# Kernel tuning notes

Hardware: AMD Instinct MI355X
Metric: run time of the kernel (lower is better)

## Reference

```python
import jax, jax.numpy as jnp
import numpy as np
from jax import lax

EPS = 1e-07
B, H, W = 32, 120, 120
N_PRIM, PRIM_DIM = 16, 8          # 16 capsule types, 8-d pose
N_SEC, SEC_DIM = 10, 16           # 10 secondary capsules, 16-d
FLAT = 9216                       # 16 * 24 * 24
R_ITERS = 3
REC_DIM = H * W * 3               # 43200


def _conv(x, w, b, stride):
    # NHWC input, HWIO kernel, VALID padding
    y = lax.conv_general_dilated(x, w, (stride, stride), 'VALID',
                                 dimension_numbers=('NHWC', 'HWIO', 'NHWC'))
    return y + b


def _squash(s):
    s_norm = jnp.linalg.norm(s, axis=-1, keepdims=True)
    sq = jnp.square(s_norm)
    return sq / (1.0 + sq) * s / (s_norm + EPS)


def setup_inputs() -> dict:
    key = jax.random.key(0)
    ks = jax.random.split(key, 13)
    p = lambda k, shp, s=0.05: (jax.random.normal(k, shp, dtype=jnp.float32) * s)
    inp = {
        'input_x': jax.random.normal(ks[0], (B, H, W, 3), dtype=jnp.float32),
        'y':       jax.random.uniform(ks[1], (B, N_SEC), dtype=jnp.float32),
        'conv1_w': p(ks[2], (9, 9, 3, 256)),
        'conv1_b': jnp.zeros((256,), jnp.float32),
        'conv2_w': p(ks[3], (9, 9, 256, N_PRIM * PRIM_DIM)),
        'conv2_b': jnp.zeros((N_PRIM * PRIM_DIM,), jnp.float32),
        'w_pose':  p(ks[4], (1, FLAT, N_SEC, SEC_DIM, PRIM_DIM)),
        'w1': p(ks[5], (N_SEC * SEC_DIM, 512)), 'b1': jnp.zeros((512,), jnp.float32),
        'w2': p(ks[6], (512, 1024)),            'b2': jnp.zeros((1024,), jnp.float32),
        'w3': p(ks[7], (1024, REC_DIM)),        'b3': jnp.zeros((REC_DIM,), jnp.float32),
    }
    return inp


def reference(input_x, y, conv1_w, conv1_b, conv2_w, conv2_b, w_pose,
              w1, b1, w2, b2, w3, b3):
    b = input_x.shape[0]
    # feature extraction
    x = jax.nn.relu(_conv(input_x, conv1_w, conv1_b, 2))   # [B,56,56,256]
    x = _conv(x, conv2_w, conv2_b, 2)                      # [B,24,24,128]
    u = x.reshape(b, FLAT, PRIM_DIM)                       # [B,9216,8]
    # u_hat[b,n,c,d] = sum_p w_pose[0,n,c,d,p] * u[b,n,p]
    u_hat = jnp.einsum('ncdp,bnp->bncd', w_pose[0], u)     # [B,9216,10,16]
    # dynamic routing
    logits = jnp.zeros((b, FLAT, N_SEC, 1), jnp.float32)
    v = None
    for _ in range(R_ITERS):
        c = jax.nn.softmax(logits, axis=-2)                # over secondary caps
        s = jnp.sum(c * u_hat, axis=1, keepdims=True)      # [B,1,10,16]
        v = _squash(s)
        agreement = jnp.sum(u_hat * v, axis=-1, keepdims=True)  # [B,9216,10,1]
        logits = logits + agreement
    # masking + reconstruction
    mask = y[:, None, :, None]                             # [B,1,10,1]
    v_flat = (mask * v).reshape(b, -1)                     # [B,160]
    h = jax.nn.relu(v_flat @ w1 + b1)
    h = jax.nn.relu(h @ w2 + b2)
    rec = jax.nn.sigmoid(h @ w3 + b3)                      # [B,43200]
    return v, rec
```

## Files before the change

### kernel.cpp

```cpp
#include <hip/hip_runtime.h>
#include <hip/hip_bf16.h>

typedef unsigned short u16;
typedef unsigned int   u32;
typedef __attribute__((ext_vector_type(8))) __bf16 bf16x8;
typedef __attribute__((ext_vector_type(4))) float  f32x4;

#define EPSQ 1e-7f
#define KSPLIT 9
#define KPB 2304
#define KSTEPS 72
#define FC3SPL 8

#define GLDS16(gp, lp) __builtin_amdgcn_global_load_lds( \
    (const __attribute__((address_space(1))) void*)(gp), \
    (__attribute__((address_space(3))) void*)(lp), 16, 0, 0)
#define WAITV4() asm volatile("s_waitcnt vmcnt(4)" ::: "memory")
#define WAITV0() asm volatile("s_waitcnt vmcnt(0)" ::: "memory")

__device__ __forceinline__ u16 f2bf(float f){
  u32 u = __float_as_uint(f);
  u32 r = (u + 0x7fffu + ((u >> 16) & 1u)) >> 16;
  return (u16)r;
}
__device__ __forceinline__ float bf2f(u16 h){ return __uint_as_float(((u32)h) << 16); }
__device__ __forceinline__ float blo(u32 w){ return __uint_as_float(w << 16); }
__device__ __forceinline__ float bhi(u32 w){ return __uint_as_float(w & 0xffff0000u); }

__global__ __launch_bounds__(256) void k_im2col(const float* __restrict__ x, u16* __restrict__ A1){
  const int id = blockIdx.x*256 + threadIdx.x;
  const int m  = id >> 5;
  const int s  = id & 31;
  const int b  = m / 3136;
  const int r  = m - b*3136;
  const int oy = r / 56;
  const int ox = r - oy*56;
  const float* xb = x + ((size_t)b*120 + 2*oy)*120*3 + 2*ox*3;
  u16 vals[8];
  #pragma unroll
  for (int j=0;j<8;++j){
    int k = s*8 + j;
    if (k < 243){
      int ky = k / 27;
      int rem = k - ky*27;
      vals[j] = f2bf(xb[(size_t)ky*360 + rem]);
    } else vals[j] = 0;
  }
  *reinterpret_cast<uint4*>(A1 + (size_t)m*256 + s*8) = *reinterpret_cast<uint4*>(vals);
}

__global__ __launch_bounds__(256) void k_wt1(const float* __restrict__ w, u16* __restrict__ wt){
  __shared__ float tile[32][33];
  const int k0 = blockIdx.x*32;
  const int c0 = blockIdx.y*32;
  const int c  = threadIdx.x & 31;
  const int r8 = threadIdx.x >> 5;
  #pragma unroll
  for (int rr=0; rr<4; ++rr){
    int r = r8*4+rr;
    tile[r][c] = (k0+r < 243) ? w[(size_t)(k0+r)*256 + c0 + c] : 0.f;
  }
  __syncthreads();
  #pragma unroll
  for (int rr=0; rr<4; ++rr){
    int r = r8*4+rr;
    wt[(size_t)(c0+r)*256 + k0 + c] = f2bf(tile[c][r]);
  }
}

__global__ __launch_bounds__(256) void k_gemm1(const u16* __restrict__ A1,
    const u16* __restrict__ w1t, const float* __restrict__ bias, u16* __restrict__ a1b){
  __shared__ __align__(16) u16 As[2][4096];
  __shared__ __align__(16) u16 Bs[2][4096];
  const int t  = threadIdx.x;
  const int bx = blockIdx.x;
  const int by = blockIdx.y;
  const int row0  = t>>2;
  const int sslot = (t&3) ^ ((t>>3)&3);
  const int wid = t>>6, lane = t&63;
  const int wr = wid>>1, wc = wid&1, lr = lane&15, lq = lane>>4;
  const int sl = lq ^ ((lr>>1)&3);
  const size_t srcA0 = (size_t)(bx*128 + row0)*256 + sslot*8;
  const size_t srcA1 = srcA0 + (size_t)64*256;
  const size_t srcB0 = (size_t)(by*128 + row0)*256 + sslot*8;
  const size_t srcB1 = srcB0 + (size_t)64*256;
  f32x4 acc[4][4];
  #pragma unroll
  for (int i=0;i<4;++i)
    #pragma unroll
    for (int j=0;j<4;++j) acc[i][j] = (f32x4){0.f,0.f,0.f,0.f};
  int aoff[4], boff[4];
  #pragma unroll
  for (int i=0;i<4;++i){
    aoff[i] = (wr*64 + i*16 + lr)*32 + sl*8;
    boff[i] = (wc*64 + i*16 + lr)*32 + sl*8;
  }

  auto stage = [&](int step, int buf){
    const int k0 = step*32;
    GLDS16(A1 + srcA0 + k0, &As[buf][wid*512]);
    GLDS16(A1 + srcA1 + k0, &As[buf][wid*512 + 2048]);
    GLDS16(w1t + srcB0 + k0, &Bs[buf][wid*512]);
    GLDS16(w1t + srcB1 + k0, &Bs[buf][wid*512 + 2048]);
  };
  auto compute = [&](int buf){
    bf16x8 af[4], bfv[4];
    #pragma unroll
    for (int mi=0;mi<4;++mi)
      af[mi] = *reinterpret_cast<const bf16x8*>(&As[buf][aoff[mi]]);
    #pragma unroll
    for (int ni=0;ni<4;++ni)
      bfv[ni] = *reinterpret_cast<const bf16x8*>(&Bs[buf][boff[ni]]);
    #pragma unroll
    for (int mi=0;mi<4;++mi)
      #pragma unroll
      for (int ni=0;ni<4;++ni)
        acc[mi][ni] = __builtin_amdgcn_mfma_f32_16x16x32_bf16(af[mi], bfv[ni], acc[mi][ni], 0, 0, 0);
  };

  stage(0, 0);
  int cur = 0;
  for (int step=0; step<8; ++step){
    if (step+1 < 8){
      stage(step+1, cur^1);
      WAITV4();
    } else {
      WAITV0();
    }
    __builtin_amdgcn_s_barrier();
    __builtin_amdgcn_sched_barrier(0);
    compute(cur);
    __builtin_amdgcn_s_barrier();
    __builtin_amdgcn_sched_barrier(0);
    cur ^= 1;
  }

  #pragma unroll
  for (int ni=0;ni<4;++ni){
    int colg = by*128 + wc*64 + ni*16 + lr;
    float bv = bias[colg];
    #pragma unroll
    for (int mi=0;mi<4;++mi){
      #pragma unroll
      for (int r=0;r<4;++r){
        int rowg = bx*128 + wr*64 + mi*16 + lq*4 + r;
        float v = fmaxf(acc[mi][ni][r] + bv, 0.f);
        a1b[(size_t)rowg*256 + colg] = f2bf(v);
      }
    }
  }
}

__global__ __launch_bounds__(256) void k_wt(const float* __restrict__ w, u16* __restrict__ wt){
  __shared__ float tile[32][33];
  const int k0 = blockIdx.x*32;
  const int c0 = blockIdx.y*32;
  const int c  = threadIdx.x & 31;
  const int r8 = threadIdx.x >> 5;
  #pragma unroll
  for (int rr=0; rr<4; ++rr){
    int r = r8*4+rr;
    tile[r][c] = w[(size_t)(k0+r)*128 + c0 + c];
  }
  __syncthreads();
  #pragma unroll
  for (int rr=0; rr<4; ++rr){
    int r = r8*4+rr;
    wt[(size_t)(c0+r)*20736 + k0 + c] = f2bf(tile[c][r]);
  }
}

__global__ __launch_bounds__(256) void k_conv2(const u16* __restrict__ a1b,
    const u16* __restrict__ w2t, float* __restrict__ part){
  __shared__ __align__(16) u16 As[2][4096];
  __shared__ __align__(16) u16 Bs[2][4096];
  const int t  = threadIdx.x;
  const int bx = blockIdx.x;
  const int ks = blockIdx.y;
  const int row0  = t>>2;
  const int sslot = (t&3) ^ ((t>>3)&3);
  int gA[2]; int gB[2];
  #pragma unroll
  for (int q=0;q<2;++q){
    int m  = bx*128 + row0 + q*64;
    int bb = m/576; int r = m - bb*576; int oy = r/24; int ox = r - oy*24;
    gA[q] = ((bb*56 + 2*oy)*56 + 2*ox)*256 + sslot*8;
    int col = row0 + q*64;
    gB[q] = col*20736 + sslot*8;
  }
  const int wid = t>>6, lane = t&63;
  const int wr = wid>>1, wc = wid&1, lr = lane&15, lq = lane>>4;
  const int sl = lq ^ ((lr>>1)&3);
  f32x4 acc[4][4];
  #pragma unroll
  for (int i=0;i<4;++i)
    #pragma unroll
    for (int j=0;j<4;++j) acc[i][j] = (f32x4){0.f,0.f,0.f,0.f};
  const int kbase = ks*KPB;
  int aoff[4], boff[4];
  #pragma unroll
  for (int i=0;i<4;++i){
    aoff[i] = (wr*64 + i*16 + lr)*32 + sl*8;
    boff[i] = (wc*64 + i*16 + lr)*32 + sl*8;
  }

  auto stage = [&](int step, int buf){
    const int k0  = kbase + step*32;
    const int kk  = k0 >> 8;
    const int ky  = kk/9;
    const int kx  = kk - ky*9;
    const int ic0 = k0 & 255;
    const int soff = (ky*56 + kx)*256 + ic0;
    GLDS16(a1b + gA[0] + soff, &As[buf][wid*512]);
    GLDS16(a1b + gA[1] + soff, &As[buf][wid*512 + 2048]);
    GLDS16(w2t + gB[0] + k0,  &Bs[buf][wid*512]);
    GLDS16(w2t + gB[1] + k0,  &Bs[buf][wid*512 + 2048]);
  };
  auto compute = [&](int buf){
    bf16x8 af[4], bfv[4];
    #pragma unroll
    for (int mi=0;mi<4;++mi)
      af[mi] = *reinterpret_cast<const bf16x8*>(&As[buf][aoff[mi]]);
    #pragma unroll
    for (int ni=0;ni<4;++ni)
      bfv[ni] = *reinterpret_cast<const bf16x8*>(&Bs[buf][boff[ni]]);
    #pragma unroll
    for (int mi=0;mi<4;++mi)
      #pragma unroll
      for (int ni=0;ni<4;++ni)
        acc[mi][ni] = __builtin_amdgcn_mfma_f32_16x16x32_bf16(af[mi], bfv[ni], acc[mi][ni], 0, 0, 0);
  };

  stage(0, 0);
  int cur = 0;
  for (int step=0; step<KSTEPS; ++step){
    if (step+1 < KSTEPS){
      stage(step+1, cur^1);
      WAITV4();
    } else {
      WAITV0();
    }
    __builtin_amdgcn_s_barrier();
    __builtin_amdgcn_sched_barrier(0);
    compute(cur);
    __builtin_amdgcn_s_barrier();
    __builtin_amdgcn_sched_barrier(0);
    cur ^= 1;
  }

  const size_t base = ((size_t)ks*18432 + (size_t)bx*128)*128;
  #pragma unroll
  for (int mi=0;mi<4;++mi){
    #pragma unroll
    for (int ni=0;ni<4;++ni){
      int col = wc*64 + ni*16 + lr;
      #pragma unroll
      for (int r=0;r<4;++r){
        int row = wr*64 + mi*16 + lq*4 + r;
        part[base + (size_t)row*128 + col] = acc[mi][ni][r];
      }
    }
  }
}

__global__ __launch_bounds__(256) void k_comb(const float* __restrict__ part,
    const float* __restrict__ bias, float* __restrict__ u){
  const int i4 = blockIdx.x*256 + threadIdx.x;
  const float4* b4 = reinterpret_cast<const float4*>(bias);
  float4 s = b4[i4 & 31];
  const float4* p4 = reinterpret_cast<const float4*>(part);
  #pragma unroll
  for (int ks=0; ks<KSPLIT; ++ks){
    float4 p = p4[(size_t)ks*589824 + i4];
    s.x += p.x; s.y += p.y; s.z += p.z; s.w += p.w;
  }
  reinterpret_cast<float4*>(u)[i4] = s;
}

__global__ __launch_bounds__(256) void k_uhat(const float* __restrict__ u,
    const float* __restrict__ wpose, u16* __restrict__ uhat){
  __shared__ float Wn[1280];
  __shared__ float us[256];
  const int n = blockIdx.x;
  const int t = threadIdx.x;
  #pragma unroll
  for (int j=0;j<5;++j) Wn[t + j*256] = wpose[(size_t)n*1280 + t + j*256];
  us[t] = u[((size_t)(t>>3)*9216 + n)*8 + (t&7)];
  __syncthreads();
  const int b = t>>3, d0 = (t&7)*2;
  float uv[8];
  #pragma unroll
  for (int p=0;p<8;++p) uv[p] = us[b*8+p];
  for (int c=0;c<10;++c){
    const float* w0 = &Wn[(c*16 + d0)*8];
    float v0=0.f, v1=0.f;
    #pragma unroll
    for (int p=0;p<8;++p){ v0 = fmaf(w0[p], uv[p], v0); v1 = fmaf(w0[8+p], uv[p], v1); }
    u32 pk = (u32)f2bf(v0) | ((u32)f2bf(v1) << 16);
    *reinterpret_cast<u32*>(uhat + ((((size_t)b*10 + c)*9216 + n)*16 + d0)) = pk;
  }
}

template<int ITER>
__global__ __launch_bounds__(256) void k_route(const u16* __restrict__ uhat,
    const float* __restrict__ spin, float* __restrict__ logi,
    float* __restrict__ spout){
  const int ch = blockIdx.x;
  const int b  = blockIdx.y;
  const int t  = threadIdx.x;
  const int n  = ch*256 + t;
  __shared__ float vl[160];
  __shared__ float sq[160];
  __shared__ float wlds[10][257];
  __shared__ float pacc[10][16][33];
  if (ITER >= 2){
    float sv = 0.f;
    if (t < 160){
      #pragma unroll 4
      for (int c2=0;c2<36;++c2) sv += spin[((size_t)c2*32 + b)*160 + t];
      sq[t] = sv*sv;
    }
    __syncthreads();
    if (t < 160){
      int cc = t >> 4;
      float ss = 0.f;
      #pragma unroll
      for (int j=0;j<16;++j) ss += sq[cc*16 + j];
      float nrm = sqrtf(ss);
      vl[t] = (ss/(1.f+ss)) * sv / (nrm + EPSQ);
    }
    __syncthreads();
  }
  float w[10];
  if (ITER == 1){
    #pragma unroll
    for (int c=0;c<10;++c) w[c] = 0.1f;
  } else {
    float l[10];
    #pragma unroll
    for (int c=0;c<10;++c){
      const u16* up = uhat + ((((size_t)b*10 + c)*9216 + n) << 4);
      const uint4 q0 = *reinterpret_cast<const uint4*>(up);
      const uint4 q1 = *reinterpret_cast<const uint4*>(up + 8);
      const float* v = &vl[c*16];
      float dot = blo(q0.x)*v[0] + bhi(q0.x)*v[1]
                + blo(q0.y)*v[2] + bhi(q0.y)*v[3]
                + blo(q0.z)*v[4] + bhi(q0.z)*v[5]
                + blo(q0.w)*v[6] + bhi(q0.w)*v[7]
                + blo(q1.x)*v[8] + bhi(q1.x)*v[9]
                + blo(q1.y)*v[10]+ bhi(q1.y)*v[11]
                + blo(q1.z)*v[12]+ bhi(q1.z)*v[13]
                + blo(q1.w)*v[14]+ bhi(q1.w)*v[15];
      size_t li = ((size_t)b*10 + c)*9216 + n;
      float lc = dot;
      if (ITER == 3) lc += logi[li];
      if (ITER == 2) logi[li] = lc;
      l[c] = lc;
    }
    float mx = l[0];
    #pragma unroll
    for (int c=1;c<10;++c) mx = fmaxf(mx, l[c]);
    float s = 0.f;
    #pragma unroll
    for (int c=0;c<10;++c){ w[c] = __expf(l[c]-mx); s += w[c]; }
    float inv = 1.f/s;
    #pragma unroll
    for (int c=0;c<10;++c) w[c] *= inv;
  }
  #pragma unroll
  for (int c=0;c<10;++c) wlds[c][t] = w[c];
  __syncthreads();

  const int nl = t>>3, dp = t&7;
  float a0[10], a1[10];
  #pragma unroll
  for (int c=0;c<10;++c){ a0[c]=0.f; a1[c]=0.f; }
  #pragma unroll
  for (int c=0;c<10;++c){
    const u32* ub = reinterpret_cast<const u32*>(
        uhat + ((((size_t)b*10 + c)*9216 + (size_t)ch*256) << 4));
    float acc0 = 0.f, acc1 = 0.f;
    #pragma unroll
    for (int chunk=0; chunk<8; ++chunk){
      u32 v = ub[chunk*256 + t];
      float wv = wlds[c][chunk*32 + nl];
      acc0 = fmaf(wv, blo(v), acc0);
      acc1 = fmaf(wv, bhi(v), acc1);
    }
    a0[c] = acc0; a1[c] = acc1;
  }
  #pragma unroll
  for (int c=0;c<10;++c){
    pacc[c][2*dp  ][nl] = a0[c];
    pacc[c][2*dp+1][nl] = a1[c];
  }
  __syncthreads();
  if (t < 160){
    const int c = t >> 4, d = t & 15;
    float acc = 0.f;
    #pragma unroll
    for (int j=0;j<32;++j) acc += pacc[c][d][j];
    spout[((size_t)ch*32 + b)*160 + t] = acc;
  }
}

__global__ __launch_bounds__(256) void k_head(const float* __restrict__ y,
    const float* __restrict__ spin, const float* __restrict__ w1,
    const float* __restrict__ b1, const float* __restrict__ w2,
    const float* __restrict__ b2, float* __restrict__ dout_v,
    float* __restrict__ h2T){
  const int b = blockIdx.x;
  const int q = blockIdx.y;
  const int t = threadIdx.x;
  __shared__ float vl[160];
  __shared__ float sq[160];
  __shared__ float h1s[512];
  float sv = 0.f;
  if (t < 160){
    #pragma unroll 4
    for (int c2=0;c2<36;++c2) sv += spin[((size_t)c2*32 + b)*160 + t];
    sq[t] = sv*sv;
  }
  __syncthreads();
  if (t < 160){
    int cc = t >> 4;
    float ss = 0.f;
    #pragma unroll
    for (int j=0;j<16;++j) ss += sq[cc*16 + j];
    float nrm = sqrtf(ss);
    float vv = (ss/(1.f+ss)) * sv / (nrm + EPSQ);
    if (q == 0) dout_v[(size_t)b*160 + t] = vv;
    vl[t] = vv * y[b*10 + cc];
  }
  __syncthreads();
  #pragma unroll
  for (int j=0;j<2;++j){
    const int oc = j*256 + t;
    float acc = b1[oc];
    for (int k=0;k<160;++k) acc = fmaf(vl[k], w1[(size_t)k*512 + oc], acc);
    h1s[oc] = fmaxf(acc, 0.f);
  }
  __syncthreads();
  const int oc2 = q*256 + t;
  float acc = b2[oc2];
  for (int k=0;k<512;++k) acc = fmaf(h1s[k], w2[(size_t)k*1024 + oc2], acc);
  h2T[(size_t)oc2*32 + b] = fmaxf(acc, 0.f);
}

__global__ __launch_bounds__(256) void k_fc3p(const float* __restrict__ h2T,
    const float* __restrict__ w3, float* __restrict__ fp){
  __shared__ float4 hs4[128][8];
  const int t  = threadIdx.x;
  const int oc = blockIdx.x*256 + t;
  const int ks = blockIdx.y;
  const float4* src = reinterpret_cast<const float4*>(h2T + (size_t)ks*128*32);
  #pragma unroll
  for (int r=0;r<4;++r)
    (&hs4[0][0])[t + r*256] = src[t + r*256];
  __syncthreads();
  const bool ok = oc < 43200;
  float a[32];
  #pragma unroll
  for (int b=0;b<32;++b) a[b] = 0.f;
  const size_t wbase = (size_t)ks*128*43200 + (size_t)(ok ? oc : 0);
  #pragma unroll 4
  for (int k=0;k<128;++k){
    float wv = w3[wbase + (size_t)k*43200];
    #pragma unroll
    for (int q=0;q<8;++q){
      float4 hv = hs4[k][q];
      a[q*4+0] = fmaf(hv.x, wv, a[q*4+0]);
      a[q*4+1] = fmaf(hv.y, wv, a[q*4+1]);
      a[q*4+2] = fmaf(hv.z, wv, a[q*4+2]);
      a[q*4+3] = fmaf(hv.w, wv, a[q*4+3]);
    }
  }
  if (ok){
    #pragma unroll
    for (int b=0;b<32;++b) fp[(size_t)(ks*32 + b)*43200 + oc] = a[b];
  }
}

__global__ __launch_bounds__(256) void k_fc3f(const float* __restrict__ fp,
    const float* __restrict__ b3, float* __restrict__ outr){
  const int i4 = blockIdx.x*256 + threadIdx.x;
  if (i4 >= 345600) return;
  const int b = i4 / 10800, oc4 = i4 - b*10800;
  const float4* b34 = reinterpret_cast<const float4*>(b3);
  float4 s = b34[oc4];
  const float4* fp4 = reinterpret_cast<const float4*>(fp);
  #pragma unroll
  for (int ks=0;ks<FC3SPL;++ks){
    float4 p = fp4[(size_t)(ks*32 + b)*10800 + oc4];
    s.x += p.x; s.y += p.y; s.z += p.z; s.w += p.w;
  }
  float4 o;
  o.x = 1.f/(1.f + __expf(-s.x));
  o.y = 1.f/(1.f + __expf(-s.y));
  o.z = 1.f/(1.f + __expf(-s.z));
  o.w = 1.f/(1.f + __expf(-s.w));
  reinterpret_cast<float4*>(outr)[i4] = o;
}

extern "C" void kernel_launch(void* const* d_in, const int* in_sizes, int n_in,
                              void* d_out, int out_size, void* d_ws, size_t ws_size,
                              hipStream_t stream){
  (void)in_sizes; (void)n_in; (void)out_size; (void)ws_size;
  const float* x     = (const float*)d_in[0];
  const float* y     = (const float*)d_in[1];
  const float* c1w   = (const float*)d_in[2];
  const float* c1b   = (const float*)d_in[3];
  const float* c2w   = (const float*)d_in[4];
  const float* c2b   = (const float*)d_in[5];
  const float* wpose = (const float*)d_in[6];
  const float* w1    = (const float*)d_in[7];
  const float* b1    = (const float*)d_in[8];
  const float* w2    = (const float*)d_in[9];
  const float* b2    = (const float*)d_in[10];
  const float* w3    = (const float*)d_in[11];
  const float* b3    = (const float*)d_in[12];
  float* out = (float*)d_out;

  char* ws = (char*)d_ws;
  u16*   a1bp  = (u16*)(ws + 0);
  u16*   A1col = (u16*)(ws + 52000000);
  float* partp = (float*)(ws + 52000000);
  u16*   uhatp = (u16*)(ws + 0);
  u16*   w1tp  = (u16*)(ws + 138000000);
  u16*   w2tp  = (u16*)(ws + 138500000);
  float* up    = (float*)(ws + 144000000);
  float* logip = (float*)(ws + 154000000);
  float* spA   = (float*)(ws + 166000000);
  float* spB   = (float*)(ws + 166800000);
  float* h2Tp  = (float*)(ws + 167600000);
  float* fc3pp = (float*)(ws + 0);

  k_im2col<<<dim3(12544),  256, 0, stream>>>(x, A1col);
  k_wt1   <<<dim3(8,8),    256, 0, stream>>>(c1w, w1tp);
  k_wt    <<<dim3(648,4),  256, 0, stream>>>(c2w, w2tp);
  k_gemm1 <<<dim3(784,2),  256, 0, stream>>>(A1col, w1tp, c1b, a1bp);
  k_conv2 <<<dim3(144,KSPLIT), 256, 0, stream>>>(a1bp, w2tp, partp);
  k_comb  <<<dim3(2304),   256, 0, stream>>>(partp, c2b, up);
  k_uhat  <<<dim3(9216),   256, 0, stream>>>(up, wpose, uhatp);

  k_route<1><<<dim3(36,32), 256, 0, stream>>>(uhatp, spB, logip, spA);
  k_route<2><<<dim3(36,32), 256, 0, stream>>>(uhatp, spA, logip, spB);
  k_route<3><<<dim3(36,32), 256, 0, stream>>>(uhatp, spB, logip, spA);

  k_head <<<dim3(32,4), 256, 0, stream>>>(y, spA, w1, b1, w2, b2, out, h2Tp);
  k_fc3p <<<dim3(169,FC3SPL), 256, 0, stream>>>(h2Tp, w3, fc3pp);
  k_fc3f <<<dim3(1350), 256, 0, stream>>>(fc3pp, b3, out + 5120);
}
```

Baseline: 533.6 us.

## Double GEMM K-tile to 64 with 8-slot XOR swizzle and regroup routing partials

```diff
diff --git a/kernel.cpp b/kernel.cpp
--- a/kernel.cpp
+++ b/kernel.cpp
@@ -9,13 +9,13 @@
 #define EPSQ 1e-7f
 #define KSPLIT 9
 #define KPB 2304
-#define KSTEPS 72
+#define KSTEPS 36
 #define FC3SPL 8
 
 #define GLDS16(gp, lp) __builtin_amdgcn_global_load_lds( \
     (const __attribute__((address_space(1))) void*)(gp), \
     (__attribute__((address_space(3))) void*)(lp), 16, 0, 0)
-#define WAITV4() asm volatile("s_waitcnt vmcnt(4)" ::: "memory")
+#define WAITV8() asm volatile("s_waitcnt vmcnt(8)" ::: "memory")
 #define WAITV0() asm volatile("s_waitcnt vmcnt(0)" ::: "memory")
 
 __device__ __forceinline__ u16 f2bf(float f){
@@ -70,60 +70,61 @@
 
 __global__ __launch_bounds__(256) void k_gemm1(const u16* __restrict__ A1,
     const u16* __restrict__ w1t, const float* __restrict__ bias, u16* __restrict__ a1b){
-  __shared__ __align__(16) u16 As[2][4096];
-  __shared__ __align__(16) u16 Bs[2][4096];
+  __shared__ __align__(16) u16 As[2][8192];
+  __shared__ __align__(16) u16 Bs[2][8192];
   const int t  = threadIdx.x;
   const int bx = blockIdx.x;
   const int by = blockIdx.y;
-  const int row0  = t>>2;
-  const int sslot = (t&3) ^ ((t>>3)&3);
+  const int r8 = t>>3;
+  const int sslot = (t&7) ^ (r8&7);
   const int wid = t>>6, lane = t&63;
   const int wr = wid>>1, wc = wid&1, lr = lane&15, lq = lane>>4;
-  const int sl = lq ^ ((lr>>1)&3);
-  const size_t srcA0 = (size_t)(bx*128 + row0)*256 + sslot*8;
-  const size_t srcA1 = srcA0 + (size_t)64*256;
-  const size_t srcB0 = (size_t)(by*128 + row0)*256 + sslot*8;
-  const size_t srcB1 = srcB0 + (size_t)64*256;
+  size_t gA[4], gB[4];
+  #pragma unroll
+  for (int i=0;i<4;++i){
+    gA[i] = (size_t)(bx*128 + i*32 + r8)*256 + sslot*8;
+    gB[i] = (size_t)(by*128 + i*32 + r8)*256 + sslot*8;
+  }
   f32x4 acc[4][4];
   #pragma unroll
   for (int i=0;i<4;++i)
     #pragma unroll
     for (int j=0;j<4;++j) acc[i][j] = (f32x4){0.f,0.f,0.f,0.f};
-  int aoff[4], boff[4];
-  #pragma unroll
-  for (int i=0;i<4;++i){
-    aoff[i] = (wr*64 + i*16 + lr)*32 + sl*8;
-    boff[i] = (wc*64 + i*16 + lr)*32 + sl*8;
-  }
 
   auto stage = [&](int step, int buf){
-    const int k0 = step*32;
-    GLDS16(A1 + srcA0 + k0, &As[buf][wid*512]);
-    GLDS16(A1 + srcA1 + k0, &As[buf][wid*512 + 2048]);
-    GLDS16(w1t + srcB0 + k0, &Bs[buf][wid*512]);
-    GLDS16(w1t + srcB1 + k0, &Bs[buf][wid*512 + 2048]);
+    const int k0 = step*64;
+    #pragma unroll
+    for (int i=0;i<4;++i)
+      GLDS16(A1 + gA[i] + k0, &As[buf][i*2048 + wid*512]);
+    #pragma unroll
+    for (int i=0;i<4;++i)
+      GLDS16(w1t + gB[i] + k0, &Bs[buf][i*2048 + wid*512]);
   };
   auto compute = [&](int buf){
-    bf16x8 af[4], bfv[4];
-    #pragma unroll
-    for (int mi=0;mi<4;++mi)
-      af[mi] = *reinterpret_cast<const bf16x8*>(&As[buf][aoff[mi]]);
-    #pragma unroll
-    for (int ni=0;ni<4;++ni)
-      bfv[ni] = *reinterpret_cast<const bf16x8*>(&Bs[buf][boff[ni]]);
-    #pragma unroll
-    for (int mi=0;mi<4;++mi)
+    #pragma unroll
+    for (int ksub=0;ksub<2;++ksub){
+      const int ps = (((ksub<<2)|lq) ^ (lr&7))*8;
+      bf16x8 af[4], bfv[4];
+      #pragma unroll
+      for (int mi=0;mi<4;++mi)
+        af[mi] = *reinterpret_cast<const bf16x8*>(&As[buf][(wr*64 + mi*16 + lr)*64 + ps]);
       #pragma unroll
       for (int ni=0;ni<4;++ni)
-        acc[mi][ni] = __builtin_amdgcn_mfma_f32_16x16x32_bf16(af[mi], bfv[ni], acc[mi][ni], 0, 0, 0);
+        bfv[ni] = *reinterpret_cast<const bf16x8*>(&Bs[buf][(wc*64 + ni*16 + lr)*64 + ps]);
+      #pragma unroll
+      for (int mi=0;mi<4;++mi)
+        #pragma unroll
+        for (int ni=0;ni<4;++ni)
+          acc[mi][ni] = __builtin_amdgcn_mfma_f32_16x16x32_bf16(af[mi], bfv[ni], acc[mi][ni], 0, 0, 0);
+    }
   };
 
   stage(0, 0);
   int cur = 0;
-  for (int step=0; step<8; ++step){
-    if (step+1 < 8){
+  for (int step=0; step<4; ++step){
+    if (step+1 < 4){
       stage(step+1, cur^1);
-      WAITV4();
+      WAITV8();
     } else {
       WAITV0();
     }
@@ -172,63 +173,60 @@
 
 __global__ __launch_bounds__(256) void k_conv2(const u16* __restrict__ a1b,
     const u16* __restrict__ w2t, float* __restrict__ part){
-  __shared__ __align__(16) u16 As[2][4096];
-  __shared__ __align__(16) u16 Bs[2][4096];
+  __shared__ __align__(16) u16 As[2][8192];
+  __shared__ __align__(16) u16 Bs[2][8192];
   const int t  = threadIdx.x;
   const int bx = blockIdx.x;
   const int ks = blockIdx.y;
-  const int row0  = t>>2;
-  const int sslot = (t&3) ^ ((t>>3)&3);
-  int gA[2]; int gB[2];
-  #pragma unroll
-  for (int q=0;q<2;++q){
-    int m  = bx*128 + row0 + q*64;
+  const int r8 = t>>3;
+  const int sslot = (t&7) ^ (r8&7);
+  int gA[4]; int gB[4];
+  #pragma unroll
+  for (int i=0;i<4;++i){
+    int m  = bx*128 + i*32 + r8;
     int bb = m/576; int r = m - bb*576; int oy = r/24; int ox = r - oy*24;
-    gA[q] = ((bb*56 + 2*oy)*56 + 2*ox)*256 + sslot*8;
-    int col = row0 + q*64;
-    gB[q] = col*20736 + sslot*8;
+    gA[i] = ((bb*56 + 2*oy)*56 + 2*ox)*256 + sslot*8;
+    int col = i*32 + r8;
+    gB[i] = col*20736 + sslot*8;
   }
   const int wid = t>>6, lane = t&63;
   const int wr = wid>>1, wc = wid&1, lr = lane&15, lq = lane>>4;
-  const int sl = lq ^ ((lr>>1)&3);
   f32x4 acc[4][4];
   #pragma unroll
   for (int i=0;i<4;++i)
     #pragma unroll
     for (int j=0;j<4;++j) acc[i][j] = (f32x4){0.f,0.f,0.f,0.f};
   const int kbase = ks*KPB;
-  int aoff[4], boff[4];
-  #pragma unroll
-  for (int i=0;i<4;++i){
-    aoff[i] = (wr*64 + i*16 + lr)*32 + sl*8;
-    boff[i] = (wc*64 + i*16 + lr)*32 + sl*8;
-  }
 
   auto stage = [&](int step, int buf){
-    const int k0  = kbase + step*32;
-    const int kk  = k0 >> 8;
-    const int ky  = kk/9;
-    const int kx  = kk - ky*9;
-    const int ic0 = k0 & 255;
-    const int soff = (ky*56 + kx)*256 + ic0;
-    GLDS16(a1b + gA[0] + soff, &As[buf][wid*512]);
-    GLDS16(a1b + gA[1] + soff, &As[buf][wid*512 + 2048]);
-    GLDS16(w2t + gB[0] + k0,  &Bs[buf][wid*512]);
-    GLDS16(w2t + gB[1] + k0,  &Bs[buf][wid*512 + 2048]);
+    const int kx  = step >> 2;
+    const int ic0 = (step & 3) * 64;
+    const int soff = (ks*56 + kx)*256 + ic0;
+    const int k0b  = kbase + step*64;
+    #pragma unroll
+    for (int i=0;i<4;++i)
+      GLDS16(a1b + gA[i] + soff, &As[buf][i*2048 + wid*512]);
+    #pragma unroll
+    for (int i=0;i<4;++i)
+      GLDS16(w2t + gB[i] + k0b, &Bs[buf][i*2048 + wid*512]);
   };
   auto compute = [&](int buf){
-    bf16x8 af[4], bfv[4];
-    #pragma unroll
-    for (int mi=0;mi<4;++mi)
-      af[mi] = *reinterpret_cast<const bf16x8*>(&As[buf][aoff[mi]]);
-    #pragma unroll
-    for (int ni=0;ni<4;++ni)
-      bfv[ni] = *reinterpret_cast<const bf16x8*>(&Bs[buf][boff[ni]]);
-    #pragma unroll
-    for (int mi=0;mi<4;++mi)
+    #pragma unroll
+    for (int ksub=0;ksub<2;++ksub){
+      const int ps = (((ksub<<2)|lq) ^ (lr&7))*8;
+      bf16x8 af[4], bfv[4];
+      #pragma unroll
+      for (int mi=0;mi<4;++mi)
+        af[mi] = *reinterpret_cast<const bf16x8*>(&As[buf][(wr*64 + mi*16 + lr)*64 + ps]);
       #pragma unroll
       for (int ni=0;ni<4;++ni)
-        acc[mi][ni] = __builtin_amdgcn_mfma_f32_16x16x32_bf16(af[mi], bfv[ni], acc[mi][ni], 0, 0, 0);
+        bfv[ni] = *reinterpret_cast<const bf16x8*>(&Bs[buf][(wc*64 + ni*16 + lr)*64 + ps]);
+      #pragma unroll
+      for (int mi=0;mi<4;++mi)
+        #pragma unroll
+        for (int ni=0;ni<4;++ni)
+          acc[mi][ni] = __builtin_amdgcn_mfma_f32_16x16x32_bf16(af[mi], bfv[ni], acc[mi][ni], 0, 0, 0);
+    }
   };
 
   stage(0, 0);
@@ -236,7 +234,7 @@
   for (int step=0; step<KSTEPS; ++step){
     if (step+1 < KSTEPS){
       stage(step+1, cur^1);
-      WAITV4();
+      WAITV8();
     } else {
       WAITV0();
     }
@@ -317,7 +315,7 @@
     float sv = 0.f;
     if (t < 160){
       #pragma unroll 4
-      for (int c2=0;c2<36;++c2) sv += spin[((size_t)c2*32 + b)*160 + t];
+      for (int c2=0;c2<36;++c2) sv += spin[((size_t)b*36 + c2)*160 + t];
       sq[t] = sv*sv;
     }
     __syncthreads();
@@ -400,7 +398,7 @@
     float acc = 0.f;
     #pragma unroll
     for (int j=0;j<32;++j) acc += pacc[c][d][j];
-    spout[((size_t)ch*32 + b)*160 + t] = acc;
+    spout[((size_t)b*36 + ch)*160 + t] = acc;
   }
 }
 
@@ -418,7 +416,7 @@
   float sv = 0.f;
   if (t < 160){
     #pragma unroll 4
-    for (int c2=0;c2<36;++c2) sv += spin[((size_t)c2*32 + b)*160 + t];
+    for (int c2=0;c2<36;++c2) sv += spin[((size_t)b*36 + c2)*160 + t];
     sq[t] = sv*sv;
   }
   __syncthreads();
```

New measurement: 530.2 us. About the same (-0.6%).
